# Kernel optimization log

Hardware: AMD Instinct MI355X
Metric: run time of the kernel (lower is better)

## Reference

```python
import jax, jax.numpy as jnp
import numpy as np

NEG_SLOPE = 0.2  # LeakyReLU slope used throughout the torch module
K = 20           # hard-coded in Net.__init__ (self.k = 20)


def leaky(x):
    return jnp.where(x >= 0, x, NEG_SLOPE * x)


def setup_inputs() -> dict:
    key = jax.random.key(0)
    ks = jax.random.split(key, 11)
    B, N = 8, 2048
    Cin, Co = 6, 64  # AGConv(3*2, 64, 3*2)
    x = jax.random.normal(ks[0], (B, 3, N), dtype=jnp.float32)
    # 1x1 conv weights (bias=False in the torch code)
    W0 = jax.random.normal(ks[1], (Co, Cin), dtype=jnp.float32) / np.sqrt(Cin)      # AGConv.conv0
    W1 = jax.random.normal(ks[2], (Co * Cin, Co), dtype=jnp.float32) / np.sqrt(Co)  # AGConv.conv1
    Wc = jax.random.normal(ks[3], (3, Co), dtype=jnp.float32) / np.sqrt(Co)         # Net.conv1
    # inference-mode BatchNorm folded to per-channel scale/shift
    bn0_s = jax.random.uniform(ks[4], (Co,), minval=0.5, maxval=1.5)
    bn0_b = 0.1 * jax.random.normal(ks[5], (Co,))
    bn1_s = jax.random.uniform(ks[6], (Co,), minval=0.5, maxval=1.5)
    bn1_b = 0.1 * jax.random.normal(ks[7], (Co,))
    bnc_s = jax.random.uniform(ks[8], (3,), minval=0.5, maxval=1.5)
    bnc_b = 0.1 * jax.random.normal(ks[9], (3,))
    return dict(x=x, W0=W0, bn0_s=bn0_s, bn0_b=bn0_b, W1=W1, bn1_s=bn1_s,
                bn1_b=bn1_b, Wc=Wc, bnc_s=bnc_s, bnc_b=bnc_b)


def reference(x, W0, bn0_s, bn0_b, W1, bn1_s, bn1_b, Wc, bnc_s, bnc_b):
    B, C, N = x.shape  # [B, 3, N]
    xt = jnp.transpose(x, (0, 2, 1))  # [B, N, 3]
    inner = jnp.einsum('bci,bcj->bij', x, x)          # [B, N, N]
    xx = jnp.sum(x * x, axis=1)                       # [B, N]
    pd = 2.0 * inner - xx[:, :, None] - xx[:, None, :]
    _, idx = jax.lax.top_k(pd, K)                     # [B, N, K] int32
    # get_graph_feature: gather neighbor coords, concat (nbr - ctr, ctr)
    nbr = xt[jnp.arange(B)[:, None, None], idx]       # [B, N, K, 3]
    ctr = jnp.broadcast_to(xt[:, :, None, :], (B, N, K, C))
    e = jnp.concatenate([nbr - ctr, ctr], axis=-1)    # [B, N, K, 6]
    # p == e here since both get_graph_feature calls use the same input & idx
    # AGConv: generate per-edge [64,6] weights from e, apply to e
    y = leaky(jnp.einsum('bnki,oi->bnko', e, W0) * bn0_s + bn0_b)   # [B, N, K, 64]
    y = jnp.einsum('bnko,po->bnkp', y, W1).reshape(B, N, K, 64, 6)  # per-edge weight mats
    out = jnp.einsum('bnkoi,bnki->bnko', y, e)                      # adaptive conv
    out = leaky(out * bn1_s + bn1_b)                                # [B, N, K, 64]
    # max-pool aggregate over neighbors
    x1 = jnp.max(out, axis=2)                                       # [B, N, 64]
    # Net.conv1: 1x1 conv 64->3 + BN + leaky
    z = leaky(jnp.einsum('bno,co->bnc', x1, Wc) * bnc_s + bnc_b)    # [B, N, 3]
    return jnp.transpose(z, (0, 2, 1))                              # [B, 3, N]
```

## Files before the change

kernel.cpp:

```cpp
#include <hip/hip_runtime.h>

#define NEGSLOPE 0.2f
#define NINF (-3.4e38f)

typedef _Float16 half8 __attribute__((ext_vector_type(8)));
typedef float f32x4 __attribute__((ext_vector_type(4)));
typedef unsigned long long u64;

#define YSTRIDE 72

__device__ __forceinline__ half8 h8zero() {
    half8 z;
#pragma unroll
    for (int i = 0; i < 8; ++i) z[i] = (_Float16)0.f;
    return z;
}

template <int CTRL>
__device__ __forceinline__ unsigned dpp_movm(unsigned v) {
    return (unsigned)__builtin_amdgcn_update_dpp(-1, (int)v, CTRL, 0xF, 0xF, false);
}

__global__ __launch_bounds__(256) void topk_kernel(
    const float* __restrict__ x, int* __restrict__ idx_out,
    const float* __restrict__ w1, _Float16* __restrict__ w1g,
    const float* __restrict__ w0, _Float16* __restrict__ w0f,
    f32x4* __restrict__ xt) {
    if (blockIdx.x >= 4096) {
        const int pid = blockIdx.x - 4096;
        int tid = pid * 256 + threadIdx.x;
#pragma unroll
        for (int it = 0; it < 12; ++it, tid += 2048) {
            int j = tid & 7;
            int L = (tid >> 3) & 63;
            int r = tid >> 9;
            int t4 = r & 3;
            int ks = r >> 2;
            int q = L >> 4, c = L & 15;
            int i = ks >> 1;
            int o = 32 * (ks & 1) + 8 * q + j;
            int u = 16 * t4 + c;
            w1g[tid] = (_Float16)w1[(u * 6 + i) * 64 + o];
        }
        if (pid == 0) {
#pragma unroll
            for (int s = 0; s < 2; ++s) {
                int t2 = threadIdx.x * 2 + s;
                int r8 = t2 >> 3, j = t2 & 7;
                w0f[t2] = (j < 6) ? (_Float16)w0[r8 * 6 + j] : (_Float16)0.f;
            }
        }
        int base = pid * 2048;
#pragma unroll
        for (int it = 0; it < 8; ++it) {
            int i = base + it * 256 + threadIdx.x;
            int bb = i >> 11, n = i & 2047;
            const float* xbp = x + bb * 6144;
            xt[i] = (f32x4){xbp[n], xbp[2048 + n], xbp[4096 + n], 0.f};
        }
        return;
    }

    const int wave = threadIdx.x >> 6;
    const int lane = threadIdx.x & 63;
    const int row = blockIdx.x * 4 + wave;
    const int b = row >> 11;
    const int n = row & 2047;
    const float* xb = x + b * 6144;
    const float xn0 = xb[n];
    const float xn1 = xb[2048 + n];
    const float xn2 = xb[4096 + n];

    unsigned skh[32];
    u64 g1 = ~0ull, g2 = ~0ull;

#pragma unroll
    for (int t = 0; t < 32; ++t) {
        const int j = t * 64 + lane;
        const float dx = xb[j] - xn0;
        const float dy = xb[2048 + j] - xn1;
        const float dz = xb[4096 + j] - xn2;
        const float d = dx * dx + dy * dy + dz * dz;
        const unsigned s = __float_as_uint(d);
        skh[t] = s;
        const u64 cand = ((u64)s << 32) | (unsigned)j;
        const bool lt = cand < g1;
        const u64 dem = lt ? g1 : cand;
        g1 = lt ? cand : g1;
        if (dem < g2) g2 = dem;
    }

    const int out_base = row * 20;

    if (lane == 0) idx_out[out_base] = n;
    const bool selfLane = (lane == (n & 63));
    unsigned zmask = selfLane ? (1u << (n >> 6)) : 0u;
    if (selfLane) { g1 = g2; g2 = ~0ull; }

    for (int k = 1; k < 20; ++k) {
        unsigned m = (unsigned)(g1 >> 32);
        { unsigned o = dpp_movm<0x111>(m); m = o < m ? o : m; }
        { unsigned o = dpp_movm<0x112>(m); m = o < m ? o : m; }
        { unsigned o = dpp_movm<0x114>(m); m = o < m ? o : m; }
        { unsigned o = dpp_movm<0x118>(m); m = o < m ? o : m; }
        { unsigned o = dpp_movm<0x142>(m); m = o < m ? o : m; }
        { unsigned o = dpp_movm<0x143>(m); m = o < m ? o : m; }
        const unsigned K = (unsigned)__builtin_amdgcn_readlane((int)m, 63);
        const u64 ball = __ballot((unsigned)(g1 >> 32) == K);
        const int Ls = __ffsll(ball) - 1;
        const int bj = __builtin_amdgcn_readlane((int)(unsigned)g1, Ls);
        if (lane == 0) idx_out[out_base + k] = bj;

        if (k < 19) {
            const bool isL = (lane == Ls);
            zmask |= isL ? (1u << (bj >> 6)) : 0u;
            if (isL) { g1 = g2; g2 = ~0ull; }
            const unsigned h1 = (unsigned)(g1 >> 32);
            if (__builtin_amdgcn_readlane((int)h1, Ls) == -1) {
                u64 n1 = ~0ull, n2 = ~0ull;
#pragma unroll
                for (int t = 0; t < 32; ++t) {
                    const unsigned sv =
                        ((zmask >> t) & 1u) ? 0xFFFFFFFFu : skh[t];
                    const u64 cc = ((u64)sv << 32) | (unsigned)(t * 64 + lane);
                    const bool lt = cc < n1;
                    const u64 dem = lt ? n1 : cc;
                    n1 = lt ? cc : n1;
                    if (dem < n2) n2 = dem;
                }
                g1 = n1;
                g2 = n2;
            }
        }
    }
}

__global__ __launch_bounds__(128, 3) void mlp_mfma(
    const f32x4* __restrict__ xt, const int* __restrict__ idx,
    const _Float16* __restrict__ w0f, const float* __restrict__ bn0s,
    const float* __restrict__ bn0b, const _Float16* __restrict__ w1g,
    const float* __restrict__ bn1s, const float* __restrict__ bn1b,
    const float* __restrict__ wc, const float* __restrict__ bncs,
    const float* __restrict__ bncb, float* __restrict__ out) {
    __shared__ __align__(16) _Float16 yL[2][80 * YSTRIDE];
    __shared__ __align__(16) half8 eL[2][80];
    const int wave = threadIdx.x >> 6;
    const int lane = threadIdx.x & 63;
    const int q = lane >> 4, c = lane & 15;
    const int gw = blockIdx.x * 2 + wave;
    const int b = gw >> 9;
    const int P0 = (gw & 511) * 4;
    _Float16* yw = yL[wave];
    half8* ew = eL[wave];
    const f32x4* xtb = xt + (b << 11);

    {
        const int k = lane >> 2, pt = lane & 3;
        const int n = P0 + pt;
        const int j = idx[(b * 2048 + n) * 20 + k];
        const f32x4 cc = xtb[n];
        const f32x4 nb = xtb[j];
        half8 ev;
        ev[0] = (_Float16)(nb[0] - cc[0]); ev[1] = (_Float16)(nb[1] - cc[1]);
        ev[2] = (_Float16)(nb[2] - cc[2]); ev[3] = (_Float16)cc[0];
        ev[4] = (_Float16)cc[1];           ev[5] = (_Float16)cc[2];
        ev[6] = (_Float16)0.f;             ev[7] = (_Float16)0.f;
        ew[lane] = ev;
    }
    if (lane < 16) {
        const int el = 64 + lane;
        const int k = el >> 2, pt = el & 3;
        const int n = P0 + pt;
        const int j = idx[(b * 2048 + n) * 20 + k];
        const f32x4 cc = xtb[n];
        const f32x4 nb = xtb[j];
        half8 ev;
        ev[0] = (_Float16)(nb[0] - cc[0]); ev[1] = (_Float16)(nb[1] - cc[1]);
        ev[2] = (_Float16)(nb[2] - cc[2]); ev[3] = (_Float16)cc[0];
        ev[4] = (_Float16)cc[1];           ev[5] = (_Float16)cc[2];
        ev[6] = (_Float16)0.f;             ev[7] = (_Float16)0.f;
        ew[el] = ev;
    }

    const half8* w0f8 = (const half8*)w0f;
    const half8 z8 = h8zero();
    half8 B1[4];
    float s0v[4], b0v[4];
#pragma unroll
    for (int nt = 0; nt < 4; ++nt) {
        const half8 v = w0f8[nt * 16 + c];
        B1[nt] = (q == 0) ? v : z8;
        s0v[nt] = bn0s[16 * nt + c];
        b0v[nt] = bn0b[16 * nt + c];
    }
#pragma unroll
    for (int mt = 0; mt < 5; ++mt) {
        const half8 ev = ew[16 * mt + c];
        const half8 Ae = (q == 0) ? ev : z8;
        const int ebase = 16 * mt + 4 * q;
#pragma unroll
        for (int nt = 0; nt < 4; ++nt) {
            f32x4 D = {0.f, 0.f, 0.f, 0.f};
            D = __builtin_amdgcn_mfma_f32_16x16x32_f16(Ae, B1[nt], D, 0, 0, 0);
#pragma unroll
            for (int r = 0; r < 4; ++r) {
                float v = D[r] * s0v[nt] + b0v[nt];
                v = fmaxf(v, NEGSLOPE * v);
                const int edge = ebase + r;
                yw[edge * YSTRIDE + ((16 * nt + c) ^ (edge & 0x38))] =
                    (_Float16)v;
            }
        }
    }

    const half8* w1g8 = (const half8*)w1g;

    f32x4 acc[5][4];
#pragma unroll
    for (int mm = 0; mm < 5; ++mm)
#pragma unroll
        for (int t4 = 0; t4 < 4; ++t4) acc[mm][t4] = (f32x4){0.f, 0.f, 0.f, 0.f};

#pragma unroll 1
    for (int i6 = 0; i6 < 6; ++i6) {
        _Float16 es[5];
#pragma unroll
        for (int mm = 0; mm < 5; ++mm)
            es[mm] = ((const _Float16*)(ew + 16 * mm + c))[i6];
#pragma unroll
        for (int ks2 = 0; ks2 < 2; ++ks2) {
            const int ks = 2 * i6 + ks2;
            half8 B[4];
#pragma unroll
            for (int t4 = 0; t4 < 4; ++t4)
                B[t4] = w1g8[(ks * 4 + t4) * 64 + lane];
#pragma unroll
            for (int mm = 0; mm < 5; ++mm) {
                const int rrow = 16 * mm + c;
                const half8 Af = *(const half8*)&yw[rrow * YSTRIDE +
                                                    ((32 * ks2 + 8 * q) ^ (rrow & 0x38))];
                const half8 An = Af * es[mm];
#pragma unroll
                for (int t4 = 0; t4 < 4; ++t4)
                    acc[mm][t4] = __builtin_amdgcn_mfma_f32_16x16x32_f16(
                        An, B[t4], acc[mm][t4], 0, 0, 0);
            }
        }
    }

    float bs1[4], bb1[4];
#pragma unroll
    for (int t4 = 0; t4 < 4; ++t4) {
        bs1[t4] = bn1s[16 * t4 + c];
        bb1[t4] = bn1b[16 * t4 + c];
    }

    float x1[4][4];
#pragma unroll
    for (int r = 0; r < 4; ++r)
#pragma unroll
        for (int t4 = 0; t4 < 4; ++t4) {
            float v = NINF;
#pragma unroll
            for (int mm = 0; mm < 5; ++mm) {
                float w = acc[mm][t4][r] * bs1[t4] + bb1[t4];
                w = fmaxf(w, NEGSLOPE * w);
                v = fmaxf(v, w);
            }
            v = fmaxf(v, __shfl_xor(v, 16, 64));
            v = fmaxf(v, __shfl_xor(v, 32, 64));
            x1[r][t4] = v;
        }

    float wcv[3][4];
#pragma unroll
    for (int co = 0; co < 3; ++co)
#pragma unroll
        for (int t4 = 0; t4 < 4; ++t4) wcv[co][t4] = wc[co * 64 + 16 * t4 + c];

    float part[4][3];
#pragma unroll
    for (int r = 0; r < 4; ++r)
#pragma unroll
        for (int co = 0; co < 3; ++co) {
            float s = x1[r][0] * wcv[co][0] + x1[r][1] * wcv[co][1] +
                      x1[r][2] * wcv[co][2] + x1[r][3] * wcv[co][3];
#pragma unroll
            for (int d = 1; d < 16; d <<= 1) s += __shfl_xor(s, d, 64);
            part[r][co] = s;
        }

    if (c == 0 && q < 3) {
        const float sc = bncs[q], bc = bncb[q];
#pragma unroll
        for (int r = 0; r < 4; ++r) {
            float z = part[r][q] * sc + bc;
            z = fmaxf(z, NEGSLOPE * z);
            out[(b * 3 + q) * 2048 + P0 + r] = z;
        }
    }
}

extern "C" void kernel_launch(void* const* d_in, const int* in_sizes, int n_in,
                              void* d_out, int out_size, void* d_ws, size_t ws_size,
                              hipStream_t stream) {
    const float* x    = (const float*)d_in[0];
    const float* W0   = (const float*)d_in[1];
    const float* bn0s = (const float*)d_in[2];
    const float* bn0b = (const float*)d_in[3];
    const float* W1   = (const float*)d_in[4];
    const float* bn1s = (const float*)d_in[5];
    const float* bn1b = (const float*)d_in[6];
    const float* Wc   = (const float*)d_in[7];
    const float* bncs = (const float*)d_in[8];
    const float* bncb = (const float*)d_in[9];

    _Float16* w1g = (_Float16*)d_ws;
    _Float16* w0f = (_Float16*)((char*)d_ws + 49152);
    f32x4* xt = (f32x4*)((char*)d_ws + 65536);
    int* idx = (int*)((char*)d_ws + 327680);

    topk_kernel<<<4104, 256, 0, stream>>>(x, idx, W1, w1g, W0, w0f, xt);
    mlp_mfma<<<2048, 128, 0, stream>>>(xt, idx, w0f, bn0s, bn0b, w1g,
                                       bn1s, bn1b, Wc, bncs, bncb,
                                       (float*)d_out);
}
```

Before: 151.9 us.

## Keep top-3 per lane in kNN and double-buffer W1 fragment loads

The top-k kernel now tracks three best candidates per lane instead of two, so a lane's full 32-element rescan is needed less often during the 19 selection rounds. The cost is an extra compare/select chain per element in the initial and rescan passes. The MFMA loop is restructured to prefetch the next W1 B-fragments from global memory while the current MFMAs run, hiding load latency at the price of more live VGPRs under a (128,3) launch bound.

```diff
diff --git a/kernel.cpp b/kernel.cpp
--- a/kernel.cpp
+++ b/kernel.cpp
@@ -72,7 +72,7 @@
     const float xn2 = xb[4096 + n];
 
     unsigned skh[32];
-    u64 g1 = ~0ull, g2 = ~0ull;
+    u64 g1 = ~0ull, g2 = ~0ull, g3 = ~0ull;
 
 #pragma unroll
     for (int t = 0; t < 32; ++t) {
@@ -84,10 +84,14 @@
         const unsigned s = __float_as_uint(d);
         skh[t] = s;
         const u64 cand = ((u64)s << 32) | (unsigned)j;
-        const bool lt = cand < g1;
-        const u64 dem = lt ? g1 : cand;
-        g1 = lt ? cand : g1;
-        if (dem < g2) g2 = dem;
+        const bool lt1 = cand < g1;
+        const u64 i1 = lt1 ? cand : g1;
+        const u64 c2 = lt1 ? g1 : cand;
+        const bool lt2 = c2 < g2;
+        const u64 i2 = lt2 ? c2 : g2;
+        const u64 c3 = lt2 ? g2 : c2;
+        const u64 i3 = c3 < g3 ? c3 : g3;
+        g1 = i1; g2 = i2; g3 = i3;
     }
 
     const int out_base = row * 20;
@@ -95,7 +99,7 @@
     if (lane == 0) idx_out[out_base] = n;
     const bool selfLane = (lane == (n & 63));
     unsigned zmask = selfLane ? (1u << (n >> 6)) : 0u;
-    if (selfLane) { g1 = g2; g2 = ~0ull; }
+    if (selfLane) { g1 = g2; g2 = g3; g3 = ~0ull; }
 
     for (int k = 1; k < 20; ++k) {
         unsigned m = (unsigned)(g1 >> 32);
@@ -114,22 +118,25 @@
         if (k < 19) {
             const bool isL = (lane == Ls);
             zmask |= isL ? (1u << (bj >> 6)) : 0u;
-            if (isL) { g1 = g2; g2 = ~0ull; }
+            if (isL) { g1 = g2; g2 = g3; g3 = ~0ull; }
             const unsigned h1 = (unsigned)(g1 >> 32);
             if (__builtin_amdgcn_readlane((int)h1, Ls) == -1) {
-                u64 n1 = ~0ull, n2 = ~0ull;
+                u64 n1 = ~0ull, n2 = ~0ull, n3 = ~0ull;
 #pragma unroll
                 for (int t = 0; t < 32; ++t) {
                     const unsigned sv =
                         ((zmask >> t) & 1u) ? 0xFFFFFFFFu : skh[t];
                     const u64 cc = ((u64)sv << 32) | (unsigned)(t * 64 + lane);
-                    const bool lt = cc < n1;
-                    const u64 dem = lt ? n1 : cc;
-                    n1 = lt ? cc : n1;
-                    if (dem < n2) n2 = dem;
+                    const bool lt1 = cc < n1;
+                    const u64 i1 = lt1 ? cc : n1;
+                    const u64 c2 = lt1 ? n1 : cc;
+                    const bool lt2 = c2 < n2;
+                    const u64 i2 = lt2 ? c2 : n2;
+                    const u64 c3 = lt2 ? n2 : c2;
+                    const u64 i3 = c3 < n3 ? c3 : n3;
+                    n1 = i1; n2 = i2; n3 = i3;
                 }
-                g1 = n1;
-                g2 = n2;
+                g1 = n1; g2 = n2; g3 = n3;
             }
         }
     }
@@ -221,30 +228,50 @@
 #pragma unroll
         for (int t4 = 0; t4 < 4; ++t4) acc[mm][t4] = (f32x4){0.f, 0.f, 0.f, 0.f};
 
+    half8 B0[4];
+#pragma unroll
+    for (int t4 = 0; t4 < 4; ++t4) B0[t4] = w1g8[t4 * 64 + lane];
+
 #pragma unroll 1
-    for (int i6 = 0; i6 < 6; ++i6) {
+    for (int kp = 0; kp < 6; ++kp) {
         _Float16 es[5];
 #pragma unroll
         for (int mm = 0; mm < 5; ++mm)
-            es[mm] = ((const _Float16*)(ew + 16 * mm + c))[i6];
-#pragma unroll
-        for (int ks2 = 0; ks2 < 2; ++ks2) {
-            const int ks = 2 * i6 + ks2;
-            half8 B[4];
+            es[mm] = ((const _Float16*)(ew + 16 * mm + c))[kp];
+
+        half8 Bn[4];
+#pragma unroll
+        for (int t4 = 0; t4 < 4; ++t4)
+            Bn[t4] = w1g8[((2 * kp + 1) * 4 + t4) * 64 + lane];
+
+#pragma unroll
+        for (int mm = 0; mm < 5; ++mm) {
+            const int rrow = 16 * mm + c;
+            const half8 Af =
+                *(const half8*)&yw[rrow * YSTRIDE + ((8 * q) ^ (rrow & 0x38))];
+            const half8 An = Af * es[mm];
 #pragma unroll
             for (int t4 = 0; t4 < 4; ++t4)
-                B[t4] = w1g8[(ks * 4 + t4) * 64 + lane];
-#pragma unroll
-            for (int mm = 0; mm < 5; ++mm) {
-                const int rrow = 16 * mm + c;
-                const half8 Af = *(const half8*)&yw[rrow * YSTRIDE +
-                                                    ((32 * ks2 + 8 * q) ^ (rrow & 0x38))];
-                const half8 An = Af * es[mm];
-#pragma unroll
-                for (int t4 = 0; t4 < 4; ++t4)
-                    acc[mm][t4] = __builtin_amdgcn_mfma_f32_16x16x32_f16(
-                        An, B[t4], acc[mm][t4], 0, 0, 0);
-            }
+                acc[mm][t4] = __builtin_amdgcn_mfma_f32_16x16x32_f16(
+                    An, B0[t4], acc[mm][t4], 0, 0, 0);
+        }
+
+        if (kp < 5) {
+#pragma unroll
+            for (int t4 = 0; t4 < 4; ++t4)
+                B0[t4] = w1g8[((2 * kp + 2) * 4 + t4) * 64 + lane];
+        }
+
+#pragma unroll
+        for (int mm = 0; mm < 5; ++mm) {
+            const int rrow = 16 * mm + c;
+            const half8 Af =
+                *(const half8*)&yw[rrow * YSTRIDE + ((32 + 8 * q) ^ (rrow & 0x38))];
+            const half8 An = Af * es[mm];
+#pragma unroll
+            for (int t4 = 0; t4 < 4; ++t4)
+                acc[mm][t4] = __builtin_amdgcn_mfma_f32_16x16x32_f16(
+                    An, Bn[t4], acc[mm][t4], 0, 0, 0);
         }
     }
 
```

Result: slower. 160.9 us (+5.9%).

## Replace iterative wave-argmin top-k with packed-key per-lane top-4 plus bitonic sort

Applied to the files above, without the earlier changes.

Packs a truncated squared distance and the point index into a single 32-bit key. Each lane keeps a sorted top-4 while scanning its 32 candidates, then a wave-wide bitonic sort over 256 keys yields the top 20 directly. This removes the 19 serial argmin rounds, the 64-bit compares and the periodic rescans. A ballot detects when some lane's 5th-best could have reached the top 20, and those rows fall back to a 20-pass recompute. Truncating the low 11 mantissa bits changes tie-breaking and ordering for near-equal distances, which may reorder neighbours compared with the reference.

```diff
diff --git a/kernel.cpp b/kernel.cpp
--- a/kernel.cpp
+++ b/kernel.cpp
@@ -15,6 +15,9 @@
     for (int i = 0; i < 8; ++i) z[i] = (_Float16)0.f;
     return z;
 }
+
+__device__ __forceinline__ unsigned umin(unsigned a, unsigned b) { return a < b ? a : b; }
+__device__ __forceinline__ unsigned umax(unsigned a, unsigned b) { return a > b ? a : b; }
 
 template <int CTRL>
 __device__ __forceinline__ unsigned dpp_movm(unsigned v) {
@@ -71,8 +74,9 @@
     const float xn1 = xb[2048 + n];
     const float xn2 = xb[4096 + n];
 
-    unsigned skh[32];
-    u64 g1 = ~0ull, g2 = ~0ull;
+    unsigned r0 = 0xFFFFFFFFu, r1 = 0xFFFFFFFFu;
+    unsigned r2 = 0xFFFFFFFFu, r3 = 0xFFFFFFFFu;
+    unsigned g5k = 0xFFFFFFFFu;
 
 #pragma unroll
     for (int t = 0; t < 32; ++t) {
@@ -81,56 +85,92 @@
         const float dy = xb[2048 + j] - xn1;
         const float dz = xb[4096 + j] - xn2;
         const float d = dx * dx + dy * dy + dz * dz;
-        const unsigned s = __float_as_uint(d);
-        skh[t] = s;
-        const u64 cand = ((u64)s << 32) | (unsigned)j;
-        const bool lt = cand < g1;
-        const u64 dem = lt ? g1 : cand;
-        g1 = lt ? cand : g1;
-        if (dem < g2) g2 = dem;
-    }
+        unsigned p = (__float_as_uint(d) & 0xFFFFF800u) | (unsigned)j;
+        unsigned q0 = umin(r0, p); p = umax(r0, p); r0 = q0;
+        unsigned q1 = umin(r1, p); p = umax(r1, p); r1 = q1;
+        unsigned q2 = umin(r2, p); p = umax(r2, p); r2 = q2;
+        unsigned q3 = umin(r3, p); p = umax(r3, p); r3 = q3;
+        g5k = umin(g5k, p);
+    }
+
+    if (lane & 1) {
+        unsigned t0 = r0; r0 = r3; r3 = t0;
+        unsigned t1 = r1; r1 = r2; r2 = t1;
+    }
+
+#define CROSS(DL, KK)                                                         \
+    {                                                                         \
+        const bool asc = ((lane >> ((KK) - 2)) & 1) == 0;                     \
+        const bool low = (lane & (DL)) == 0;                                  \
+        const bool selmin = (asc == low);                                     \
+        const unsigned p0 = (unsigned)__shfl_xor((int)r0, (DL), 64);          \
+        const unsigned p1 = (unsigned)__shfl_xor((int)r1, (DL), 64);          \
+        const unsigned p2 = (unsigned)__shfl_xor((int)r2, (DL), 64);          \
+        const unsigned p3 = (unsigned)__shfl_xor((int)r3, (DL), 64);          \
+        r0 = selmin ? umin(r0, p0) : umax(r0, p0);                            \
+        r1 = selmin ? umin(r1, p1) : umax(r1, p1);                            \
+        r2 = selmin ? umin(r2, p2) : umax(r2, p2);                            \
+        r3 = selmin ? umin(r3, p3) : umax(r3, p3);                            \
+    }
+#define INLANE(KK)                                                            \
+    {                                                                         \
+        const bool asc = ((lane >> ((KK) - 2)) & 1) == 0;                     \
+        { unsigned lo = umin(r0, r2), hi = umax(r0, r2);                      \
+          r0 = asc ? lo : hi; r2 = asc ? hi : lo; }                           \
+        { unsigned lo = umin(r1, r3), hi = umax(r1, r3);                      \
+          r1 = asc ? lo : hi; r3 = asc ? hi : lo; }                           \
+        { unsigned lo = umin(r0, r1), hi = umax(r0, r1);                      \
+          r0 = asc ? lo : hi; r1 = asc ? hi : lo; }                           \
+        { unsigned lo = umin(r2, r3), hi = umax(r2, r3);                      \
+          r2 = asc ? lo : hi; r3 = asc ? hi : lo; }                           \
+    }
+
+    CROSS(1, 3)  INLANE(3)
+    CROSS(2, 4)  CROSS(1, 4)  INLANE(4)
+    CROSS(4, 5)  CROSS(2, 5)  CROSS(1, 5)  INLANE(5)
+    CROSS(8, 6)  CROSS(4, 6)  CROSS(2, 6)  CROSS(1, 6)  INLANE(6)
+    CROSS(16, 7) CROSS(8, 7)  CROSS(4, 7)  CROSS(2, 7)  CROSS(1, 7)  INLANE(7)
+    CROSS(32, 8) CROSS(16, 8) CROSS(8, 8)  CROSS(4, 8)  CROSS(2, 8)  CROSS(1, 8)
+    INLANE(8)
+#undef CROSS
+#undef INLANE
 
     const int out_base = row * 20;
-
-    if (lane == 0) idx_out[out_base] = n;
-    const bool selfLane = (lane == (n & 63));
-    unsigned zmask = selfLane ? (1u << (n >> 6)) : 0u;
-    if (selfLane) { g1 = g2; g2 = ~0ull; }
-
-    for (int k = 1; k < 20; ++k) {
-        unsigned m = (unsigned)(g1 >> 32);
-        { unsigned o = dpp_movm<0x111>(m); m = o < m ? o : m; }
-        { unsigned o = dpp_movm<0x112>(m); m = o < m ? o : m; }
-        { unsigned o = dpp_movm<0x114>(m); m = o < m ? o : m; }
-        { unsigned o = dpp_movm<0x118>(m); m = o < m ? o : m; }
-        { unsigned o = dpp_movm<0x142>(m); m = o < m ? o : m; }
-        { unsigned o = dpp_movm<0x143>(m); m = o < m ? o : m; }
-        const unsigned K = (unsigned)__builtin_amdgcn_readlane((int)m, 63);
-        const u64 ball = __ballot((unsigned)(g1 >> 32) == K);
-        const int Ls = __ffsll(ball) - 1;
-        const int bj = __builtin_amdgcn_readlane((int)(unsigned)g1, Ls);
-        if (lane == 0) idx_out[out_base + k] = bj;
-
-        if (k < 19) {
-            const bool isL = (lane == Ls);
-            zmask |= isL ? (1u << (bj >> 6)) : 0u;
-            if (isL) { g1 = g2; g2 = ~0ull; }
-            const unsigned h1 = (unsigned)(g1 >> 32);
-            if (__builtin_amdgcn_readlane((int)h1, Ls) == -1) {
-                u64 n1 = ~0ull, n2 = ~0ull;
-#pragma unroll
-                for (int t = 0; t < 32; ++t) {
-                    const unsigned sv =
-                        ((zmask >> t) & 1u) ? 0xFFFFFFFFu : skh[t];
-                    const u64 cc = ((u64)sv << 32) | (unsigned)(t * 64 + lane);
-                    const bool lt = cc < n1;
-                    const u64 dem = lt ? n1 : cc;
-                    n1 = lt ? cc : n1;
-                    if (dem < n2) n2 = dem;
-                }
-                g1 = n1;
-                g2 = n2;
-            }
+    const unsigned T20p = (unsigned)__builtin_amdgcn_readlane((int)r3, 4);
+    const u64 bad = __ballot(g5k < T20p);
+
+    if (bad == 0) {
+        if (lane < 5) {
+            int4 v;
+            v.x = (int)(r0 & 2047u); v.y = (int)(r1 & 2047u);
+            v.z = (int)(r2 & 2047u); v.w = (int)(r3 & 2047u);
+            *(int4*)(idx_out + out_base + lane * 4) = v;
+        }
+    } else {
+        unsigned Tprev = 0u;
+#pragma unroll 1
+        for (int r = 0; r < 20; ++r) {
+            unsigned best = 0xFFFFFFFFu;
+#pragma unroll
+            for (int t = 0; t < 32; ++t) {
+                const int j = t * 64 + lane;
+                const float dx = xb[j] - xn0;
+                const float dy = xb[2048 + j] - xn1;
+                const float dz = xb[4096 + j] - xn2;
+                const float d = dx * dx + dy * dy + dz * dz;
+                const unsigned p = (__float_as_uint(d) & 0xFFFFF800u) | (unsigned)j;
+                const bool ok = (r == 0) || (p > Tprev);
+                best = umin(best, ok ? p : 0xFFFFFFFFu);
+            }
+            { unsigned o = dpp_movm<0x111>(best); best = umin(best, o); }
+            { unsigned o = dpp_movm<0x112>(best); best = umin(best, o); }
+            { unsigned o = dpp_movm<0x114>(best); best = umin(best, o); }
+            { unsigned o = dpp_movm<0x118>(best); best = umin(best, o); }
+            { unsigned o = dpp_movm<0x142>(best); best = umin(best, o); }
+            { unsigned o = dpp_movm<0x143>(best); best = umin(best, o); }
+            const unsigned K = (unsigned)__builtin_amdgcn_readlane((int)best, 63);
+            if (lane == 0) idx_out[out_base + r] = (int)(K & 2047u);
+            Tprev = K;
         }
     }
 }
```

Result: faster. 136.9 us (-9.9%).
